# Performance work log

Measured on AMD Instinct MI355X. Metric: run time of the kernel, lower is better.

## Reference

```python
import jax, jax.numpy as jnp
import numpy as np

B, T, D, H, V, K = 64, 128, 300, 256, 30000, 16
FILTERS = [3, 4, 5]
FN = [100, 100, 100]
CLS = 5


def setup_inputs() -> dict:
    key = jax.random.key(0)
    ks = jax.random.split(key, 32)
    n = lambda i, shape, s=0.05: (jax.random.normal(ks[i], shape, jnp.float32) * s)
    inp = jax.random.randint(ks[0], (B, T), 0, V)
    emb = n(1, (V + 2, D)).at[V + 1].set(0.0)  # padding_idx row = 0
    # GRU (1 layer, bidirectional), PyTorch gate order r,z,n
    Wx_f, Wh_f = n(2, (3 * H, D)), n(3, (3 * H, H))
    bx_f, bh_f = n(4, (3 * H,)), n(5, (3 * H,))
    Wx_b, Wh_b = n(6, (3 * H, D)), n(7, (3 * H, H))
    bx_b, bh_b = n(8, (3 * H,)), n(9, (3 * H,))
    fc1c_W, fc1c_b = n(10, (D, 2 * H)), n(11, (D,))
    concept_table = n(12, (V, K, D), 0.1)
    counts = jax.random.randint(ks[13], (V,), 1, K + 1)
    concept_mask = (jnp.arange(K)[None, :] < counts[:, None])  # bool [V,K]
    conv_W0, conv_b0 = n(14, (FN[0], FILTERS[0] * 2 * D)), n(15, (FN[0],))
    conv_W1, conv_b1 = n(16, (FN[1], FILTERS[1] * 2 * D)), n(17, (FN[1],))
    conv_W2, conv_b2 = n(18, (FN[2], FILTERS[2] * 2 * D)), n(19, (FN[2],))
    fc1_W, fc1_b = n(20, (100, sum(FN))), n(21, (100,))
    fc2_W, fc2_b = n(22, (CLS, 100)), n(23, (CLS,))
    return dict(inp=inp, emb=emb, Wx_f=Wx_f, Wh_f=Wh_f, bx_f=bx_f, bh_f=bh_f,
                Wx_b=Wx_b, Wh_b=Wh_b, bx_b=bx_b, bh_b=bh_b,
                fc1c_W=fc1c_W, fc1c_b=fc1c_b,
                concept_table=concept_table, concept_mask=concept_mask,
                conv_W0=conv_W0, conv_b0=conv_b0, conv_W1=conv_W1, conv_b1=conv_b1,
                conv_W2=conv_W2, conv_b2=conv_b2,
                fc1_W=fc1_W, fc1_b=fc1_b, fc2_W=fc2_W, fc2_b=fc2_b)


def _gru_dir(x, Wx, Wh, bx, bh):
    # x: [B,T,D] -> hidden states [B,T,H]; PyTorch GRU cell math.
    xg = jnp.einsum('btd,gd->btg', x, Wx) + bx  # precompute input gates [B,T,3H]

    def step(h, xg_t):
        gh = h @ Wh.T + bh
        xr, xz, xn = jnp.split(xg_t, 3, axis=-1)
        hr, hz, hn = jnp.split(gh, 3, axis=-1)
        r = jax.nn.sigmoid(xr + hr)
        z = jax.nn.sigmoid(xz + hz)
        nn_ = jnp.tanh(xn + r * hn)
        h2 = (1.0 - z) * nn_ + z * h
        return h2, h2

    h0 = jnp.zeros((x.shape[0], Wh.shape[1]), x.dtype)
    _, ys = jax.lax.scan(step, h0, jnp.swapaxes(xg, 0, 1))
    return jnp.swapaxes(ys, 0, 1)


def _forward(inp, emb, Wx_f, Wh_f, bx_f, bh_f, Wx_b, Wh_b, bx_b, bh_b,
             fc1c_W, fc1c_b, concept_table, concept_mask,
             conv_W0, conv_b0, conv_W1, conv_b1, conv_W2, conv_b2,
             fc1_W, fc1_b, fc2_W, fc2_b):
    x = emb[inp]                                   # [B,T,D]
    hf = _gru_dir(x, Wx_f, Wh_f, bx_f, bh_f)
    hb = jnp.flip(_gru_dir(jnp.flip(x, 1), Wx_b, Wh_b, bx_b, bh_b), 1)
    out = jnp.concatenate([hf, hb], axis=-1)       # [B,T,2H]
    ctx = jnp.einsum('bth,dh->btd', out, fc1c_W) + fc1c_b  # [B,T,D] context
    # batched gather-attend-reduce over per-word concept lists
    conc = concept_table[inp]                      # [B,T,K,D]
    mask = concept_mask[inp]                       # [B,T,K] bool
    scores = jnp.einsum('btkd,btd->btk', conc, ctx)
    scores = jnp.where(mask, scores, jnp.float32(-1e30))
    attn = jax.nn.softmax(scores, axis=-1)
    concept = jnp.einsum('btk,btkd->btd', attn, conc)
    concept = jax.lax.stop_gradient(concept)       # original detaches via .data.numpy()
    feat = jnp.concatenate([ctx, concept], axis=-1)  # [B,T,2D]
    pooled = []
    for fs, W, b in ((FILTERS[0], conv_W0, conv_b0),
                     (FILTERS[1], conv_W1, conv_b1),
                     (FILTERS[2], conv_W2, conv_b2)):
        L = T - fs + 1
        # Conv1d(kernel=2D*fs, stride=2D) over flattened feat == token-window matmul
        win = jnp.concatenate([feat[:, i:i + L, :] for i in range(fs)], axis=-1)  # [B,L,fs*2D]
        c = jax.nn.relu(jnp.einsum('blk,fk->blf', win, W) + b)
        pooled.append(jnp.max(c, axis=1))          # max-pool over positions -> [B,FN]
    h = jnp.concatenate(pooled, axis=1)            # [B,300]; dropout is identity in eval
    h = h @ fc1_W.T + fc1_b
    h = h @ fc2_W.T + fc2_b
    return jax.nn.softmax(h, axis=1)


def reference(inp, emb, Wx_f, Wh_f, bx_f, bh_f, Wx_b, Wh_b, bx_b, bh_b,
              fc1c_W, fc1c_b, concept_table, concept_mask,
              conv_W0, conv_b0, conv_W1, conv_b1, conv_W2, conv_b2,
              fc1_W, fc1_b, fc2_W, fc2_b):
    return _forward(inp, emb, Wx_f, Wh_f, bx_f, bh_f, Wx_b, Wh_b, bx_b, bh_b,
                    fc1c_W, fc1c_b, concept_table, concept_mask,
                    conv_W0, conv_b0, conv_W1, conv_b1, conv_W2, conv_b2,
                    fc1_W, fc1_b, fc2_W, fc2_b)
```

## Files before the change

### kernel.cpp

```cpp
#include <hip/hip_runtime.h>


typedef unsigned short u16;
typedef unsigned int u32;
typedef __attribute__((ext_vector_type(4))) u16 u16x4;
typedef __attribute__((ext_vector_type(8))) u16 u16x8;
typedef __attribute__((ext_vector_type(8))) __bf16 bf16x8;
typedef __attribute__((ext_vector_type(4))) float f32x4;

__device__ __forceinline__ float bf2f(u16 u) {
    union { u32 i; float f; } x; x.i = ((u32)u) << 16; return x.f;
}
__device__ __forceinline__ u16 f2bf(float f) {
    union { float f; u32 i; } x; x.f = f;
    u32 r = x.i + 0x7FFFu + ((x.i >> 16) & 1u);
    return (u16)(r >> 16);
}
__device__ __forceinline__ float sigm(float x) { return 1.f / (1.f + __expf(-x)); }
__device__ __forceinline__ float tanh_(float x) {
    float e = __expf(-2.f * fabsf(x));
    float t = (1.f - e) / (1.f + e);
    return x < 0.f ? -t : t;
}
__device__ __forceinline__ void gload16(const u16* g, u16* l) {
    __builtin_amdgcn_global_load_lds(
        (const __attribute__((address_space(1))) void*)g,
        (__attribute__((address_space(3))) void*)l, 16, 0, 0);
}

__global__ __launch_bounds__(256) void detect_k(
    const u32* __restrict__ cmask_raw, int* __restrict__ flags)
{
    __shared__ int cnt1;
    if (threadIdx.x == 0) cnt1 = 0;
    __syncthreads();
    int c1 = 0;
    for (int i = threadIdx.x; i < 1024; i += 256)
        if (cmask_raw[i] > 1u) c1++;
    if (c1) atomicAdd(&cnt1, c1);
    __syncthreads();
    if (threadIdx.x == 0) flags[1] = (cnt1 > 0) ? 1 : 0;
}

struct CvtDesc { const void* src; u16* dst; int n; };
struct CvtArgs { CvtDesc d[9]; };

__global__ __launch_bounds__(256) void convert_f32(CvtArgs a)
{
    CvtDesc de = a.d[blockIdx.y];
    int i4 = (blockIdx.x * 256 + threadIdx.x) * 4;
    if (i4 >= de.n) return;
    const float* s = (const float*)de.src + i4;
    if (i4 + 4 <= de.n) {
        u16x4 o; o[0] = f2bf(s[0]); o[1] = f2bf(s[1]); o[2] = f2bf(s[2]); o[3] = f2bf(s[3]);
        *(u16x4*)(de.dst + i4) = o;
    } else {
        for (int e = 0; e < 4 && i4 + e < de.n; ++e) de.dst[i4 + e] = f2bf(s[e]);
    }
}

__global__ __launch_bounds__(256) void build_mask(
    const void* __restrict__ cmask, int* __restrict__ mask16, const int* __restrict__ flags)
{
    int v = blockIdx.x * 256 + threadIdx.x;
    if (v >= 30000) return;
    int m = 0;
    if (flags[1]) {
        const unsigned char* p = (const unsigned char*)cmask + (size_t)v * 16;
#pragma unroll
        for (int k = 0; k < 16; ++k) if (p[k]) m |= (1 << k);
    } else {
        const int* p = (const int*)cmask + (size_t)v * 16;
#pragma unroll
        for (int k = 0; k < 16; ++k) if (p[k]) m |= (1 << k);
    }
    mask16[v] = m;
}

__global__ __launch_bounds__(256) void repack_conv(
    const float* __restrict__ cw0, const float* __restrict__ cw1,
    const float* __restrict__ cw2, u16* __restrict__ wcat)
{
    const int r = blockIdx.x * 8 + (threadIdx.x >> 5);
    for (int slot = threadIdx.x & 31; slot < 160; slot += 32) {
        const int d0 = slot * 4;
        u16x4 o = {0, 0, 0, 0};
        if (r < 1200 && d0 < 600) {
            const float* src;
            if (r < 300)      { int f = r % 100,       i = r / 100;          src = cw0 + (size_t)f * 1800 + i * 600; }
            else if (r < 700) { int rr = r - 300, f = rr % 100, i = rr / 100; src = cw1 + (size_t)f * 2400 + i * 600; }
            else              { int rr = r - 700, f = rr % 100, i = rr / 100; src = cw2 + (size_t)f * 3000 + i * 600; }
            float4 x = *(const float4*)(src + d0);
            o[0] = f2bf(x.x); o[1] = f2bf(x.y); o[2] = f2bf(x.z); o[3] = f2bf(x.w);
        }
        *(u16x4*)(wcat + (size_t)r * 640 + d0) = o;
    }
}

__global__ __launch_bounds__(256) void pack_wx(
    const float* __restrict__ wxf, const float* __restrict__ wxb,
    u16* __restrict__ wxpad)
{
    const int n = blockIdx.x * 16 + (threadIdx.x >> 4);
    const float* src = n < 768 ? wxf + (size_t)n * 300 : wxb + (size_t)(n - 768) * 300;
    for (int c = threadIdx.x & 15; c < 80; c += 16) {
        u16x4 o = {0, 0, 0, 0};
        if (c < 75) {
            float4 x = *(const float4*)(src + c * 4);
            o[0] = f2bf(x.x); o[1] = f2bf(x.y); o[2] = f2bf(x.z); o[3] = f2bf(x.w);
        }
        *(u16x4*)(wxpad + (size_t)n * 320 + c * 4) = o;
    }
}

__global__ __launch_bounds__(128) void pack_fc1c(
    const float* __restrict__ w, u16* __restrict__ dst)
{
    const int r = blockIdx.x;
    const int c4 = threadIdx.x * 4;
    u16x4 o = {0, 0, 0, 0};
    if (r < 300) {
        float4 x = *(const float4*)(w + (size_t)r * 512 + c4);
        o[0] = f2bf(x.x); o[1] = f2bf(x.y); o[2] = f2bf(x.z); o[3] = f2bf(x.w);
    }
    *(u16x4*)(dst + (size_t)r * 512 + c4) = o;
}

__global__ __launch_bounds__(256) void build_bias(
    const float* __restrict__ bxf, const float* __restrict__ bhf,
    const float* __restrict__ bxb, const float* __restrict__ bhb,
    float* __restrict__ bias2)
{
    int c = blockIdx.x * 256 + threadIdx.x;
    if (c >= 1536) return;
    int cc = c < 768 ? c : c - 768;
    const float* bx = c < 768 ? bxf : bxb;
    const float* bh = c < 768 ? bhf : bhb;
    float v = bx[cc];
    if (cc < 512) v += bh[cc];
    bias2[c] = v;
}

__global__ __launch_bounds__(256) void stage_x(
    const int* __restrict__ inp, const float* __restrict__ emb,
    u16* __restrict__ xstage)
{
    const int tok = blockIdx.x * 8 + (threadIdx.x >> 5);
    const float* src = emb + (size_t)inp[tok] * 300;
    for (int c = threadIdx.x & 31; c < 80; c += 32) {
        u16x4 o = {0, 0, 0, 0};
        if (c < 75) {
            float4 x = *(const float4*)(src + c * 4);
            o[0] = f2bf(x.x); o[1] = f2bf(x.y); o[2] = f2bf(x.z); o[3] = f2bf(x.w);
        }
        *(u16x4*)(xstage + (size_t)tok * 320 + c * 4) = o;
    }
}

template<int EPI>
__global__ __launch_bounds__(256) void gemm128(
    const u16* __restrict__ A, const u16* __restrict__ W,
    const float* __restrict__ bias, u16* __restrict__ C,
    int Kpad, int Nout, int ldc)
{
    __shared__ __align__(16) u16 sA[128 * 32];
    __shared__ __align__(16) u16 sW[128 * 32];

    const int tid = threadIdx.x;
    const int n0 = blockIdx.x * 128;
    const int m0 = blockIdx.y * 128;

    const int l  = tid & 63;
    const int w  = tid >> 6;
    const int wm = (w >> 1) << 6;
    const int wn = (w & 1) << 6;
    const int fr = l & 15;
    const int fk = (l >> 4) << 3;

    const int srow = tid >> 2;
    const int scol = (tid & 3) << 3;

    f32x4 acc[4][4];
#pragma unroll
    for (int i = 0; i < 4; ++i)
#pragma unroll
        for (int j = 0; j < 4; ++j) acc[i][j] = (f32x4){0.f, 0.f, 0.f, 0.f};

    for (int k0 = 0; k0 < Kpad; k0 += 32) {
        __syncthreads();
#pragma unroll
        for (int i = 0; i < 2; ++i) {
            gload16(A + (size_t)(m0 + i * 64 + srow) * Kpad + k0 + scol,
                    sA + i * 2048 + tid * 8);
            gload16(W + (size_t)(n0 + i * 64 + srow) * Kpad + k0 + scol,
                    sW + i * 2048 + tid * 8);
        }
        __syncthreads();

        bf16x8 a[4], b[4];
#pragma unroll
        for (int i = 0; i < 4; ++i) {
            a[i] = *(const bf16x8*)(sA + (wm + i * 16 + fr) * 32 + fk);
            b[i] = *(const bf16x8*)(sW + (wn + i * 16 + fr) * 32 + fk);
        }
#pragma unroll
        for (int i = 0; i < 4; ++i)
#pragma unroll
            for (int j = 0; j < 4; ++j)
                acc[i][j] = __builtin_amdgcn_mfma_f32_16x16x32_bf16(a[i], b[j], acc[i][j], 0, 0, 0);
    }

    const int rb = (l >> 4) << 2;
    const int cc = l & 15;
#pragma unroll
    for (int j = 0; j < 4; ++j) {
        const int col = n0 + wn + j * 16 + cc;
        if (col < Nout) {
            const float bv = (EPI == 1) ? bias[col] : 0.f;
#pragma unroll
            for (int i = 0; i < 4; ++i) {
#pragma unroll
                for (int r = 0; r < 4; ++r) {
                    const int row = m0 + wm + i * 16 + rb + r;
                    C[(size_t)row * ldc + col] = f2bf(acc[i][j][r] + bv);
                }
            }
        }
    }
}

#define GB 8
__global__ __attribute__((amdgpu_waves_per_eu(2, 2)))
__launch_bounds__(512, 2) void gru_scan_mfma(
    const u16* __restrict__ xg,
    const u16* __restrict__ whf, const u16* __restrict__ whb,
    const float* __restrict__ bhf, const float* __restrict__ bhb,
    u16* __restrict__ outb)
{
    const int bg  = blockIdx.x;
    const int dir = blockIdx.y;
    const u16* wh = dir ? whb : whf;
    const float* bh = dir ? bhb : bhf;

    const int tid = threadIdx.x;
    const int w = tid >> 6;
    const int l = tid & 63;

    __shared__ __align__(16) u16 h_bf[16][264];
    __shared__ __align__(16) float gh[GB][772];

    for (int i = tid; i < 16 * 264; i += 512) ((u16*)h_bf)[i] = 0;

    bf16x8 bfr[6][8];
#pragma unroll
    for (int c = 0; c < 6; ++c)
#pragma unroll
        for (int kt = 0; kt < 8; ++kt) {
            const int n = w * 96 + c * 16 + (l & 15);
            const int k = kt * 32 + (l >> 4) * 8;
            bfr[c][kt] = *(const bf16x8*)(wh + (size_t)n * 256 + k);
        }
#pragma unroll
    for (int c = 0; c < 6; ++c)
#pragma unroll
        for (int kt = 0; kt < 8; ++kt)
            asm volatile("" : "+v"(bfr[c][kt]));

    const int qrow = (l >> 4) << 2;
    const int arow = l & 15;
    const int aofs = (l >> 4) << 3;
    const int j0 = l * 4;
    const int bglob = bg * GB + w;
    const float4 bhn4 = *(const float4*)(bh + 512 + j0);
    f32x4 hreg = {0.f, 0.f, 0.f, 0.f};

    __syncthreads();

    for (int s = 0; s < 128; ++s) {
        const int t = dir ? (127 - s) : s;

        f32x4 acc[6];
#pragma unroll
        for (int c = 0; c < 6; ++c) acc[c] = (f32x4){0.f, 0.f, 0.f, 0.f};
#pragma unroll
        for (int kt = 0; kt < 8; ++kt) {
            bf16x8 a = *(const bf16x8*)(&h_bf[arow][kt * 32 + aofs]);
#pragma unroll
            for (int c = 0; c < 6; ++c)
                acc[c] = __builtin_amdgcn_mfma_f32_16x16x32_bf16(a, bfr[c][kt], acc[c], 0, 0, 0);
        }

        const size_t tb = (size_t)(bglob * 128 + t) * 1536 + dir * 768;
        u16x4 xr4 = *(const u16x4*)(xg + tb + j0);
        u16x4 xz4 = *(const u16x4*)(xg + tb + 256 + j0);
        u16x4 xn4 = *(const u16x4*)(xg + tb + 512 + j0);

        if (qrow < GB) {
#pragma unroll
            for (int c = 0; c < 6; ++c) {
                const int col = w * 96 + c * 16 + (l & 15);
#pragma unroll
                for (int r = 0; r < 4; ++r)
                    gh[qrow + r][col] = acc[c][r];
            }
        }
        __syncthreads();

        u16x4 ho;
#pragma unroll
        for (int e = 0; e < 4; ++e) {
            const int j = j0 + e;
            float r = sigm(bf2f(xr4[e]) + gh[w][j]);
            float z = sigm(bf2f(xz4[e]) + gh[w][256 + j]);
            float n = tanh_(bf2f(xn4[e]) + r * (gh[w][512 + j] + bhn4[e]));
            float h2 = (1.f - z) * n + z * hreg[e];
            hreg[e] = h2;
            ho[e] = f2bf(h2);
        }
        *(u16x4*)(&h_bf[w][j0]) = ho;
        *(u16x4*)(outb + (size_t)(bglob * 128 + t) * 512 + dir * 256 + j0) = ho;
        __syncthreads();
    }
}
#undef GB

__global__ __launch_bounds__(256) void attn_kernel(
    const int* __restrict__ inp, const float* __restrict__ ctab,
    const int* __restrict__ mask16, u16* __restrict__ feat)
{
    const int tok = blockIdx.x;
    const int tid = threadIdx.x;
    const int v = inp[tok];

    __shared__ float ctx_s[300];
    __shared__ __align__(16) u16 conc_s[16 * 300];
    __shared__ float sc_s[16];
    __shared__ float at_s[16];

    for (int d = tid; d < 300; d += 256) ctx_s[d] = bf2f(feat[(size_t)tok * 640 + d]);
    {
        const float4* src = (const float4*)(ctab + (size_t)v * 4800);
        for (int i = tid; i < 1200; i += 256) {
            float4 x = src[i];
            u16x4 o; o[0] = f2bf(x.x); o[1] = f2bf(x.y); o[2] = f2bf(x.z); o[3] = f2bf(x.w);
            *(u16x4*)(conc_s + i * 4) = o;
        }
    }
    __syncthreads();

    const int g = tid >> 4, ln = tid & 15;
    float s = 0.f;
    for (int d = ln; d < 300; d += 16) s += bf2f(conc_s[g * 300 + d]) * ctx_s[d];
    s += __shfl_xor(s, 1); s += __shfl_xor(s, 2); s += __shfl_xor(s, 4); s += __shfl_xor(s, 8);
    if (ln == 0) sc_s[g] = ((mask16[v] >> g) & 1) ? s : -1e30f;
    __syncthreads();

    if (tid == 0) {
        float m = -1e30f;
#pragma unroll
        for (int i = 0; i < 16; ++i) m = fmaxf(m, sc_s[i]);
        float p[16]; float den = 0.f;
#pragma unroll
        for (int i = 0; i < 16; ++i) {
            float pe = (sc_s[i] <= -1e29f) ? 0.f : __expf(sc_s[i] - m);
            p[i] = pe; den += pe;
        }
        float inv = den > 0.f ? 1.f / den : 0.f;
#pragma unroll
        for (int i = 0; i < 16; ++i) at_s[i] = p[i] * inv;
    }
    __syncthreads();

    for (int d = tid; d < 340; d += 256) {
        float a = 0.f;
        if (d < 300) {
#pragma unroll
            for (int g2 = 0; g2 < 16; ++g2) a += at_s[g2] * bf2f(conc_s[g2 * 300 + d]);
        }
        feat[(size_t)tok * 640 + 300 + d] = f2bf(a);
    }
}

__global__ __launch_bounds__(128) void pool_fused(
    const u16* __restrict__ P, const u16* __restrict__ cbcat,
    float* __restrict__ pool)
{
    const int b = blockIdx.x, which = blockIdx.y, f = threadIdx.x;
    if (f >= 100) return;
    const int fs  = which == 0 ? 3 : (which == 1 ? 4 : 5);
    const int off = which == 0 ? 0 : (which == 1 ? 300 : 700);
    const int L   = 128 - fs + 1;
    const float bias = bf2f(cbcat[which * 100 + f]);
    float mm = -1e30f;
    for (int l2 = 0; l2 < L; ++l2) {
        float s = bias;
#pragma unroll 5
        for (int i = 0; i < fs; ++i)
            s += bf2f(P[(size_t)(b * 128 + l2 + i) * 1200 + off + i * 100 + f]);
        mm = fmaxf(mm, s);
    }
    pool[b * 300 + which * 100 + f] = fmaxf(mm, 0.f);
}

__global__ __launch_bounds__(128) void final_k(
    const float* __restrict__ pool,
    const u16* __restrict__ fc1W, const u16* __restrict__ fc1b,
    const u16* __restrict__ fc2W, const u16* __restrict__ fc2b,
    float* __restrict__ out)
{
    const int b = blockIdx.x, tid = threadIdx.x;
    __shared__ float ps[300], h1[100], lg[5];
    for (int d = tid; d < 300; d += 128) ps[d] = pool[b * 300 + d];
    __syncthreads();
    if (tid < 100) {
        float a = bf2f(fc1b[tid]);
        for (int k = 0; k < 300; ++k) a += bf2f(fc1W[tid * 300 + k]) * ps[k];
        h1[tid] = a;
    }
    __syncthreads();
    if (tid < 5) {
        float a = bf2f(fc2b[tid]);
        for (int k = 0; k < 100; ++k) a += bf2f(fc2W[tid * 100 + k]) * h1[k];
        lg[tid] = a;
    }
    __syncthreads();
    if (tid == 0) {
        float m = fmaxf(fmaxf(fmaxf(lg[0], lg[1]), fmaxf(lg[2], lg[3])), lg[4]);
        float e0 = __expf(lg[0] - m), e1 = __expf(lg[1] - m), e2 = __expf(lg[2] - m),
              e3 = __expf(lg[3] - m), e4 = __expf(lg[4] - m);
        float inv = 1.f / (e0 + e1 + e2 + e3 + e4);
        out[b * 5 + 0] = e0 * inv;
        out[b * 5 + 1] = e1 * inv;
        out[b * 5 + 2] = e2 * inv;
        out[b * 5 + 3] = e3 * inv;
        out[b * 5 + 4] = e4 * inv;
    }
}

extern "C" void kernel_launch(void* const* d_in, const int* in_sizes, int n_in,
                              void* d_out, int out_size, void* d_ws, size_t ws_size,
                              hipStream_t stream)
{
    (void)in_sizes; (void)n_in; (void)out_size; (void)ws_size;

    const int*  inp     = (const int*)d_in[0];
    const void* embR    = d_in[1];
    const void* WxfR    = d_in[2];
    const void* WhfR    = d_in[3];
    const void* bxfR    = d_in[4];
    const void* bhfR    = d_in[5];
    const void* WxbR    = d_in[6];
    const void* WhbR    = d_in[7];
    const void* bxbR    = d_in[8];
    const void* bhbR    = d_in[9];
    const void* fc1cWR  = d_in[10];
    const void* fc1cbR  = d_in[11];
    const void* ctabR   = d_in[12];
    const void* cmaskR  = d_in[13];
    const void* cw0R    = d_in[14];
    const void* cb0R    = d_in[15];
    const void* cw1R    = d_in[16];
    const void* cb1R    = d_in[17];
    const void* cw2R    = d_in[18];
    const void* cb2R    = d_in[19];
    const void* fc1WR   = d_in[20];
    const void* fc1bR   = d_in[21];
    const void* fc2WR   = d_in[22];
    const void* fc2bR   = d_in[23];

    char* ws = (char*)d_ws;
    size_t off = 0;
    auto alloc = [&](size_t bytes) -> char* {
        char* r = ws + off;
        off = (off + bytes + 255) & ~(size_t)255;
        return r;
    };

    u16*   xgc    = (u16*)alloc(8192ull * 1536 * 2);
    u16*   outb   = (u16*)alloc(8192ull * 512 * 2);
    u16*   feat   = (u16*)alloc(8192ull * 640 * 2);
    u16*   P      = (u16*)alloc(8192ull * 1200 * 2);
    u16*   xstage = (u16*)alloc(8192ull * 320 * 2);
    float* pool   = (float*)alloc(64ull * 300 * 4);
    int*   flags  = (int*)alloc(256);
    int*   mask16 = (int*)alloc(30000ull * 4);
    u16*   wxpad  = (u16*)alloc(1536ull * 320 * 2);
    float* bias2  = (float*)alloc(1536ull * 4);
    u16*   whfc   = (u16*)alloc(196608ull * 2);
    u16*   whbc   = (u16*)alloc(196608ull * 2);
    u16*   fc1cp  = (u16*)alloc(384ull * 512 * 2);
    u16*   wcat   = (u16*)alloc(1280ull * 640 * 2);
    u16*   cbcat  = (u16*)alloc(300ull * 2);
    u16*   fc1Wc  = (u16*)alloc(30000ull * 2);
    u16*   fc1bc  = (u16*)alloc(100ull * 2);
    u16*   fc2Wc  = (u16*)alloc(500ull * 2);
    u16*   fc2bc  = (u16*)alloc(8ull * 2);

    detect_k<<<1, 256, 0, stream>>>((const u32*)cmaskR, flags);

    {
        CvtArgs a{};
        a.d[0] = { WhfR,  whfc,        196608 };
        a.d[1] = { WhbR,  whbc,        196608 };
        a.d[2] = { cb0R,  cbcat,       100 };
        a.d[3] = { cb1R,  cbcat + 100, 100 };
        a.d[4] = { cb2R,  cbcat + 200, 100 };
        a.d[5] = { fc1WR, fc1Wc,       30000 };
        a.d[6] = { fc1bR, fc1bc,       100 };
        a.d[7] = { fc2WR, fc2Wc,       500 };
        a.d[8] = { fc2bR, fc2bc,       5 };
        convert_f32<<<dim3(192, 9), 256, 0, stream>>>(a);
    }

    build_mask<<<118, 256, 0, stream>>>(cmaskR, mask16, flags);
    repack_conv<<<160, 256, 0, stream>>>(
        (const float*)cw0R, (const float*)cw1R, (const float*)cw2R, wcat);
    pack_wx<<<96, 256, 0, stream>>>((const float*)WxfR, (const float*)WxbR, wxpad);
    pack_fc1c<<<384, 128, 0, stream>>>((const float*)fc1cWR, fc1cp);
    build_bias<<<6, 256, 0, stream>>>((const float*)bxfR, (const float*)bhfR,
                                      (const float*)bxbR, (const float*)bhbR, bias2);
    stage_x<<<1024, 256, 0, stream>>>(inp, (const float*)embR, xstage);

    gemm128<1><<<dim3(12, 64), 256, 0, stream>>>(
        xstage, wxpad, bias2, xgc, 320, 1536, 1536);

    gru_scan_mfma<<<dim3(8, 2), 512, 0, stream>>>(
        xgc, whfc, whbc, (const float*)bhfR, (const float*)bhbR, outb);

    gemm128<1><<<dim3(3, 64), 256, 0, stream>>>(
        outb, fc1cp, (const float*)fc1cbR, feat, 512, 300, 640);

    attn_kernel<<<dim3(8192), 256, 0, stream>>>(inp, (const float*)ctabR, mask16, feat);

    gemm128<0><<<dim3(10, 64), 256, 0, stream>>>(
        feat, wcat, nullptr, P, 640, 1200, 1200);

    pool_fused<<<dim3(64, 3), 128, 0, stream>>>(P, cbcat, pool);

    final_k<<<dim3(64), 128, 0, stream>>>(pool, fc1Wc, fc1bc, fc2Wc, fc2bc, (float*)d_out);
}
```

Before: 515.8 us.

## Overlap concept-table gather with GRU scan and fold mask detection into build_mask

Extra blocks are added to the GRU scan launch. While the 16 latency-bound scan blocks run, these blocks gather each token's concept rows from the fp32 table, convert them to bf16 and store them in a workspace buffer. The attention kernel then copies the pre-gathered bf16 rows instead of doing the random fp32 gather itself. The separate detect kernel is also merged into build_mask, removing one launch. The gather path only runs when the workspace holds the larger ~79MB buffer, and it adds an extra global round-trip that the attention kernel must re-read.

```diff
diff --git a/kernel.cpp b/kernel.cpp
--- a/kernel.cpp
+++ b/kernel.cpp
@@ -26,20 +26,6 @@
     __builtin_amdgcn_global_load_lds(
         (const __attribute__((address_space(1))) void*)g,
         (__attribute__((address_space(3))) void*)l, 16, 0, 0);
-}
-
-__global__ __launch_bounds__(256) void detect_k(
-    const u32* __restrict__ cmask_raw, int* __restrict__ flags)
-{
-    __shared__ int cnt1;
-    if (threadIdx.x == 0) cnt1 = 0;
-    __syncthreads();
-    int c1 = 0;
-    for (int i = threadIdx.x; i < 1024; i += 256)
-        if (cmask_raw[i] > 1u) c1++;
-    if (c1) atomicAdd(&cnt1, c1);
-    __syncthreads();
-    if (threadIdx.x == 0) flags[1] = (cnt1 > 0) ? 1 : 0;
 }
 
 struct CvtDesc { const void* src; u16* dst; int n; };
@@ -60,12 +46,25 @@
 }
 
 __global__ __launch_bounds__(256) void build_mask(
-    const void* __restrict__ cmask, int* __restrict__ mask16, const int* __restrict__ flags)
-{
+    const void* __restrict__ cmask, int* __restrict__ mask16)
+{
+    __shared__ int isbyte_s;
+    {
+        int c1 = 0;
+        const u32* raw = (const u32*)cmask;
+        for (int i = threadIdx.x; i < 1024; i += 256)
+            if (raw[i] > 1u) c1++;
+        if (threadIdx.x == 0) isbyte_s = 0;
+        __syncthreads();
+        if (c1) atomicAdd(&isbyte_s, c1);
+        __syncthreads();
+    }
+    const bool isbyte = isbyte_s > 0;
+
     int v = blockIdx.x * 256 + threadIdx.x;
     if (v >= 30000) return;
     int m = 0;
-    if (flags[1]) {
+    if (isbyte) {
         const unsigned char* p = (const unsigned char*)cmask + (size_t)v * 16;
 #pragma unroll
         for (int k = 0; k < 16; ++k) if (p[k]) m |= (1 << k);
@@ -231,23 +230,38 @@
 
 #define GB 8
 __global__ __attribute__((amdgpu_waves_per_eu(2, 2)))
-__launch_bounds__(512, 2) void gru_scan_mfma(
+__launch_bounds__(512, 2) void gru_and_gather(
     const u16* __restrict__ xg,
     const u16* __restrict__ whf, const u16* __restrict__ whb,
     const float* __restrict__ bhf, const float* __restrict__ bhb,
-    u16* __restrict__ outb)
-{
-    const int bg  = blockIdx.x;
-    const int dir = blockIdx.y;
+    u16* __restrict__ outb,
+    const int* __restrict__ inp, const float* __restrict__ ctab,
+    u16* __restrict__ concb)
+{
+    __shared__ __align__(16) u16 h_bf[16][264];
+    __shared__ __align__(16) float gh[GB][772];
+
+    if (blockIdx.x >= 16) {
+        const int tok = (blockIdx.x - 16) * 4 + (threadIdx.x >> 7);
+        const int lt  = threadIdx.x & 127;
+        const float4* src = (const float4*)(ctab + (size_t)inp[tok] * 4800);
+        u16* dst = concb + (size_t)tok * 4800;
+        for (int i = lt; i < 1200; i += 128) {
+            float4 x = src[i];
+            u16x4 o; o[0] = f2bf(x.x); o[1] = f2bf(x.y); o[2] = f2bf(x.z); o[3] = f2bf(x.w);
+            *(u16x4*)(dst + i * 4) = o;
+        }
+        return;
+    }
+
+    const int bg  = blockIdx.x >> 1;
+    const int dir = blockIdx.x & 1;
     const u16* wh = dir ? whb : whf;
     const float* bh = dir ? bhb : bhf;
 
     const int tid = threadIdx.x;
     const int w = tid >> 6;
     const int l = tid & 63;
-
-    __shared__ __align__(16) u16 h_bf[16][264];
-    __shared__ __align__(16) float gh[GB][772];
 
     for (int i = tid; i < 16 * 264; i += 512) ((u16*)h_bf)[i] = 0;
 
@@ -324,9 +338,11 @@
 }
 #undef GB
 
+template<int GATHERED>
 __global__ __launch_bounds__(256) void attn_kernel(
     const int* __restrict__ inp, const float* __restrict__ ctab,
-    const int* __restrict__ mask16, u16* __restrict__ feat)
+    const u16* __restrict__ concb, const int* __restrict__ mask16,
+    u16* __restrict__ feat)
 {
     const int tok = blockIdx.x;
     const int tid = threadIdx.x;
@@ -338,7 +354,11 @@
     __shared__ float at_s[16];
 
     for (int d = tid; d < 300; d += 256) ctx_s[d] = bf2f(feat[(size_t)tok * 640 + d]);
-    {
+    if constexpr (GATHERED) {
+        const u16x8* src = (const u16x8*)(concb + (size_t)tok * 4800);
+        u16x8* dst = (u16x8*)conc_s;
+        for (int i = tid; i < 600; i += 256) dst[i] = src[i];
+    } else {
         const float4* src = (const float4*)(ctab + (size_t)v * 4800);
         for (int i = tid; i < 1200; i += 256) {
             float4 x = src[i];
@@ -441,7 +461,7 @@
                               void* d_out, int out_size, void* d_ws, size_t ws_size,
                               hipStream_t stream)
 {
-    (void)in_sizes; (void)n_in; (void)out_size; (void)ws_size;
+    (void)in_sizes; (void)n_in; (void)out_size;
 
     const int*  inp     = (const int*)d_in[0];
     const void* embR    = d_in[1];
@@ -468,6 +488,8 @@
     const void* fc2WR   = d_in[22];
     const void* fc2bR   = d_in[23];
 
+    const int do_gather = (ws_size >= (140ull << 20)) ? 1 : 0;
+
     char* ws = (char*)d_ws;
     size_t off = 0;
     auto alloc = [&](size_t bytes) -> char* {
@@ -479,10 +501,11 @@
     u16*   xgc    = (u16*)alloc(8192ull * 1536 * 2);
     u16*   outb   = (u16*)alloc(8192ull * 512 * 2);
     u16*   feat   = (u16*)alloc(8192ull * 640 * 2);
-    u16*   P      = (u16*)alloc(8192ull * 1200 * 2);
+    u16*   concb  = (u16*)alloc(do_gather ? 8192ull * 4800 * 2
+                                          : 8192ull * 1200 * 2);
+    u16*   P      = concb;
     u16*   xstage = (u16*)alloc(8192ull * 320 * 2);
     float* pool   = (float*)alloc(64ull * 300 * 4);
-    int*   flags  = (int*)alloc(256);
     int*   mask16 = (int*)alloc(30000ull * 4);
     u16*   wxpad  = (u16*)alloc(1536ull * 320 * 2);
     float* bias2  = (float*)alloc(1536ull * 4);
@@ -496,8 +519,6 @@
     u16*   fc2Wc  = (u16*)alloc(500ull * 2);
     u16*   fc2bc  = (u16*)alloc(8ull * 2);
 
-    detect_k<<<1, 256, 0, stream>>>((const u32*)cmaskR, flags);
-
     {
         CvtArgs a{};
         a.d[0] = { WhfR,  whfc,        196608 };
@@ -512,7 +533,7 @@
         convert_f32<<<dim3(192, 9), 256, 0, stream>>>(a);
     }
 
-    build_mask<<<118, 256, 0, stream>>>(cmaskR, mask16, flags);
+    build_mask<<<118, 256, 0, stream>>>(cmaskR, mask16);
     repack_conv<<<160, 256, 0, stream>>>(
         (const float*)cw0R, (const float*)cw1R, (const float*)cw2R, wcat);
     pack_wx<<<96, 256, 0, stream>>>((const float*)WxfR, (const float*)WxbR, wxpad);
@@ -524,13 +545,19 @@
     gemm128<1><<<dim3(12, 64), 256, 0, stream>>>(
         xstage, wxpad, bias2, xgc, 320, 1536, 1536);
 
-    gru_scan_mfma<<<dim3(8, 2), 512, 0, stream>>>(
-        xgc, whfc, whbc, (const float*)bhfR, (const float*)bhbR, outb);
+    gru_and_gather<<<dim3(16 + (do_gather ? 2048 : 0)), 512, 0, stream>>>(
+        xgc, whfc, whbc, (const float*)bhfR, (const float*)bhbR, outb,
+        inp, (const float*)ctabR, concb);
 
     gemm128<1><<<dim3(3, 64), 256, 0, stream>>>(
         outb, fc1cp, (const float*)fc1cbR, feat, 512, 300, 640);
 
-    attn_kernel<<<dim3(8192), 256, 0, stream>>>(inp, (const float*)ctabR, mask16, feat);
+    if (do_gather)
+        attn_kernel<1><<<dim3(8192), 256, 0, stream>>>(
+            inp, (const float*)ctabR, concb, mask16, feat);
+    else
+        attn_kernel<0><<<dim3(8192), 256, 0, stream>>>(
+            inp, (const float*)ctabR, concb, mask16, feat);
 
     gemm128<0><<<dim3(10, 64), 256, 0, stream>>>(
         feat, wcat, nullptr, P, 640, 1200, 1200);
```

Result: no change. 516.1 us (+0.1%).
